# Performance work log

Hardware: AMD Instinct MI355X
Metric: run time of the kernel (lower is better)

Reference implementation:

```python
import jax, jax.numpy as jnp
import numpy as np
from jax import lax

EMBED_DIM = 128
N_RELATIONS = 64
N_ENTITIES = 100000
N_EDGES = 600000


def setup_inputs() -> dict:
    key = jax.random.key(0)
    k1, k2, k3, k4, k5, k6 = jax.random.split(key, 6)
    entity_emb = jax.random.normal(k1, (N_ENTITIES, EMBED_DIM), dtype=jnp.float32)
    heads = jax.random.randint(k2, (N_EDGES,), 0, N_ENTITIES)
    rels = jax.random.randint(k3, (N_EDGES,), 0, N_RELATIONS)
    tails = jax.random.randint(k4, (N_EDGES,), 0, N_ENTITIES)
    # learned params: relation embedding table (std=0.01) and square Linear weight (xavier)
    rel_embed_weight = 0.01 * jax.random.normal(k5, (N_RELATIONS, EMBED_DIM), dtype=jnp.float32)
    xavier = float(np.sqrt(6.0 / (EMBED_DIM + EMBED_DIM)))
    W = jax.random.uniform(k6, (EMBED_DIM, EMBED_DIM), dtype=jnp.float32, minval=-xavier, maxval=xavier)
    return {"entity_emb": entity_emb, "rel_embed_weight": rel_embed_weight, "W": W,
            "heads": heads, "rels": rels, "tails": tails}


def reference(entity_emb, rel_embed_weight, W, heads, rels, tails):
    n_entities = entity_emb.shape[0]
    # gather edge endpoint / relation embeddings: [E, D]
    e_h = entity_emb[heads]
    e_t = entity_emb[tails]
    e_r = rel_embed_weight[rels]
    # tanh-gated dot-product score per edge: [E]
    score = jnp.sum(e_t * jnp.tanh(e_h + e_r), axis=-1)
    # global max-shift (detached in torch) then per-head segment softmax
    score_exp = jnp.exp(score - lax.stop_gradient(jnp.max(score)))
    score_sum = jax.ops.segment_sum(score_exp, heads, num_segments=n_entities)
    attn = score_exp / (score_sum[heads] + 1e-10)
    # scatter-add attention-weighted messages back to head nodes: [N, D]
    agg = jax.ops.segment_sum(attn[:, None] * e_t, heads, num_segments=n_entities)
    # final Linear (no bias) + LeakyReLU(0.2); dropout is identity in eval mode
    out = (entity_emb + agg) @ W.T
    return jax.nn.leaky_relu(out, negative_slope=0.2)
```

## Files before the change

### kernel.cpp

```cpp
#include <hip/hip_runtime.h>
#include <math.h>

#define EMBED 128
#define BMAX 8192
#define LDSPAD 136
#define DBINS 64

#define TWO_LOG2E 2.8853900817779268f
#define DEFER_THR 32.0f

typedef __attribute__((ext_vector_type(8))) short short8;
typedef __attribute__((ext_vector_type(4))) float floatx4;

__device__ __forceinline__ float ex2(float x) { return __builtin_amdgcn_exp2f(x); }

__device__ __forceinline__ float fast_tanh2(float x) {
    float e = ex2(TWO_LOG2E * x);
    return 1.0f - 2.0f * __builtin_amdgcn_rcpf(1.0f + e);
}

__device__ __forceinline__ unsigned short f2b(float f) {
    union { float f; unsigned int u; } v; v.f = f;
    unsigned int r = v.u + 0x7FFFu + ((v.u >> 16) & 1u);
    return (unsigned short)(r >> 16);
}

__device__ __forceinline__ float b2f(short u) {
    union { float f; unsigned int i; } v;
    v.i = ((unsigned int)(unsigned short)u) << 16;
    return v.f;
}

template <int CTRL>
__device__ __forceinline__ float dpp_add_f(float x) {
    int y = __builtin_amdgcn_update_dpp(0, __float_as_int(x), CTRL, 0xF, 0xF, false);
    return x + __int_as_float(y);
}
__device__ __forceinline__ float dpp_sum16(float s) {
    s = dpp_add_f<0x121>(s);
    s = dpp_add_f<0x122>(s);
    s = dpp_add_f<0x124>(s);
    s = dpp_add_f<0x128>(s);
    return s;
}

__global__ __launch_bounds__(256) void k_cast_hist(
    const float* __restrict__ ent, const float* __restrict__ rel, const float* __restrict__ W,
    short* __restrict__ entb, short* __restrict__ relb, short* __restrict__ wb,
    const int* __restrict__ heads, int* __restrict__ cnt, int* __restrict__ ghist,
    int ngE, int ngR, int ngW, int E)
{
    if (blockIdx.x == 0 && threadIdx.x < DBINS) ghist[threadIdx.x] = 0;
    int stride = gridDim.x * 256;
    int total = ngE + ngR + ngW;
    for (int g = blockIdx.x * 256 + threadIdx.x; g < total; g += stride) {
        const float4* src; short* dst;
        if (g < ngE)            { src = (const float4*)ent + (size_t)g * 2;              dst = entb + (size_t)g * 8; }
        else if (g < ngE + ngR) { int g2 = g - ngE;       src = (const float4*)rel + (size_t)g2 * 2; dst = relb + (size_t)g2 * 8; }
        else                    { int g2 = g - ngE - ngR; src = (const float4*)W   + (size_t)g2 * 2; dst = wb   + (size_t)g2 * 8; }
        float4 a = src[0], b = src[1];
        short8 o;
        o[0] = (short)f2b(a.x); o[1] = (short)f2b(a.y); o[2] = (short)f2b(a.z); o[3] = (short)f2b(a.w);
        o[4] = (short)f2b(b.x); o[5] = (short)f2b(b.y); o[6] = (short)f2b(b.z); o[7] = (short)f2b(b.w);
        *(short8*)dst = o;
    }
    for (int e = blockIdx.x * 256 + threadIdx.x; e < E; e += stride)
        atomicAdd(cnt + heads[e], 1);
}

__global__ __launch_bounds__(1024) void k_scan1(
    const int* __restrict__ cnt, int* __restrict__ offs,
    int* __restrict__ bsum, int* __restrict__ ghist, int N)
{
    __shared__ int wsum[16];
    __shared__ int dh[DBINS];
    const int tid = threadIdx.x;
    if (tid < DBINS) dh[tid] = 0;
    int i = blockIdx.x * 1024 + tid;
    int v = (i < N) ? cnt[i] : 0;
    __syncthreads();
    if (i < N) atomicAdd(&dh[v < DBINS ? v : DBINS - 1], 1);
    int x = v;
    #pragma unroll
    for (int d = 1; d < 64; d <<= 1) {
        int y = __shfl_up(x, d, 64);
        if ((tid & 63) >= d) x += y;
    }
    if ((tid & 63) == 63) wsum[tid >> 6] = x;
    __syncthreads();
    if (tid < 16) {
        int w = wsum[tid];
        #pragma unroll
        for (int d = 1; d < 16; d <<= 1) {
            int y = __shfl_up(w, d, 16);
            if (tid >= d) w += y;
        }
        wsum[tid] = w;
    }
    __syncthreads();
    int add = (tid >= 64) ? wsum[(tid >> 6) - 1] : 0;
    int incl = x + add;
    if (i < N) offs[i] = incl - v;
    if (tid == 1023) bsum[blockIdx.x] = incl;
    if (tid < DBINS && dh[tid] > 0) atomicAdd(ghist + tid, dh[tid]);
}

__global__ __launch_bounds__(256) void k_scan23(
    int* __restrict__ offs, const int* __restrict__ bsum,
    int* __restrict__ cursor, const int* __restrict__ cnt,
    const int* __restrict__ ghist, int* __restrict__ bincur,
    int* __restrict__ order, int N, int nb)
{
    __shared__ int sb[256];
    __shared__ int ws4[4];
    __shared__ int dbs[DBINS];
    __shared__ int lcnt[DBINS];
    __shared__ int lbase[DBINS];
    const int tid = threadIdx.x;

    int v = (tid < nb) ? bsum[tid] : 0;
    int x = v;
    #pragma unroll
    for (int d = 1; d < 64; d <<= 1) {
        int y = __shfl_up(x, d, 64);
        if ((tid & 63) >= d) x += y;
    }
    if ((tid & 63) == 63) ws4[tid >> 6] = x;
    __syncthreads();
    if (tid < 4) {
        int w = ws4[tid];
        #pragma unroll
        for (int d = 1; d < 4; d <<= 1) {
            int y = __shfl_up(w, d, 4);
            if (tid >= d) w += y;
        }
        ws4[tid] = w;
    }
    __syncthreads();
    int add = (tid >= 64) ? ws4[(tid >> 6) - 1] : 0;
    sb[tid] = x + add - v;

    if (tid < 64) {
        int g = ghist[tid];
        int s = g;
        #pragma unroll
        for (int d = 1; d < 64; d <<= 1) {
            int y = __shfl_up(s, d, 64);
            if (tid >= d) s += y;
        }
        dbs[tid] = s - g;
    }
    if (tid < DBINS) lcnt[tid] = 0;
    __syncthreads();

    int i = blockIdx.x * 256 + tid;
    int deg = 0, lrank = 0;
    if (i < N) {
        int o = offs[i] + sb[i >> 10];
        offs[i] = o;
        cursor[i] = o;
        int c = cnt[i];
        deg = c < DBINS ? c : DBINS - 1;
        lrank = atomicAdd(&lcnt[deg], 1);
    }
    __syncthreads();
    if (tid < DBINS) {
        int n = lcnt[tid];
        lbase[tid] = (n > 0) ? (dbs[tid] + atomicAdd(bincur + tid, n)) : 0;
    }
    __syncthreads();
    if (i < N) order[lbase[deg] + lrank] = i;
}

__global__ __launch_bounds__(256) void k_csr(
    const int* __restrict__ heads, const int* __restrict__ rels,
    const int* __restrict__ tails, int* __restrict__ cursor,
    int2* __restrict__ tr, int E)
{
    int e = blockIdx.x * 256 + threadIdx.x;
    if (e >= E) return;
    int pos = atomicAdd(cursor + heads[e], 1);
    tr[pos] = make_int2(tails[e], rels[e]);
}

__global__ __launch_bounds__(256) void k_fused(
    const short* __restrict__ entb, const short* __restrict__ relb,
    const int* __restrict__ offs, const int* __restrict__ cnt,
    const int2* __restrict__ tr, const int* __restrict__ order,
    short* __restrict__ accb, float* __restrict__ mh, float* __restrict__ lh,
    float* __restrict__ blockmax, int N, int R)
{
    __shared__ short rl[64 * EMBED];
    const int tid = threadIdx.x;
    if (R <= 64) {
        int nch = R * 16;
        for (int i = tid; i < nch; i += 256)
            ((short8*)rl)[i] = ((const short8*)relb)[i];
    }
    __syncthreads();
    const short* relsrc = (R <= 64) ? (const short*)rl : relb;

    const int lane = tid & 15;
    int head0 = blockIdx.x * 16 + (tid >> 4);
    int head  = (head0 < N) ? order[head0] : N;
    float mt = -INFINITY;
    if (head < N) {
        int start = offs[head];
        int c     = cnt[head];
        short8 hh = *((const short8*)(entb + (size_t)head * EMBED) + lane);
        float hf[8];
        #pragma unroll
        for (int i = 0; i < 8; ++i) hf[i] = b2f(hh[i]);
        float m = -INFINITY;
        float l = 0.f;
        float acc[8] = {0,0,0,0,0,0,0,0};
        for (int base = 0; base < c; base += 16) {
            int rem = c - base;
            int mm  = rem < 16 ? rem : 16;
            int2 trv = make_int2(0, 0);
            if (lane < mm) trv = tr[start + base + lane];
            for (int j = 0; j < mm; ++j) {
                int t = __shfl(trv.x, j, 16);
                int r = __shfl(trv.y, j, 16);
                short8 vt = *((const short8*)(entb + (size_t)t * EMBED) + lane);
                short8 vr = *((const short8*)(relsrc + (size_t)r * EMBED) + lane);
                float s = 0.f;
                float vtf[8];
                #pragma unroll
                for (int i = 0; i < 8; ++i) {
                    vtf[i] = b2f(vt[i]);
                    s = fmaf(vtf[i], fast_tanh2(hf[i] + b2f(vr[i])), s);
                }
                s = dpp_sum16(s);
                mt = fmaxf(mt, s);
                float dlt = s - m;
                if (dlt > DEFER_THR) {
                    float alpha = __expf(-dlt);
                    l *= alpha;
                    #pragma unroll
                    for (int q = 0; q < 8; ++q) acc[q] *= alpha;
                    m = s;
                    dlt = 0.f;
                }
                float p = __expf(dlt);
                l += p;
                #pragma unroll
                for (int q = 0; q < 8; ++q)
                    acc[q] = fmaf(p, vtf[q], acc[q]);
            }
        }
        short8 o;
        #pragma unroll
        for (int q = 0; q < 8; ++q) o[q] = (short)f2b(acc[q]);
        *((short8*)(accb + (size_t)head * EMBED) + lane) = o;
        if (lane == 0) { mh[head] = m; lh[head] = l; }
    }
    __shared__ float smax[256];
    smax[tid] = mt;
    __syncthreads();
    for (int off = 128; off > 0; off >>= 1) {
        if (tid < off) smax[tid] = fmaxf(smax[tid], smax[tid + off]);
        __syncthreads();
    }
    if (tid == 0) blockmax[blockIdx.x] = smax[0];
}

__global__ __launch_bounds__(256) void k_maxred(
    const float* __restrict__ blockmax, float* __restrict__ Mout, int n)
{
    __shared__ float smax[256];
    float m = -INFINITY;
    for (int i = threadIdx.x; i < n; i += 256) m = fmaxf(m, blockmax[i]);
    smax[threadIdx.x] = m;
    __syncthreads();
    for (int off = 128; off > 0; off >>= 1) {
        if ((int)threadIdx.x < off)
            smax[threadIdx.x] = fmaxf(smax[threadIdx.x], smax[threadIdx.x + off]);
        __syncthreads();
    }
    if (threadIdx.x == 0) Mout[0] = smax[0];
}

__global__ __launch_bounds__(256) void k_gemm_f(
    const short* __restrict__ entb, const short* __restrict__ accb,
    const float* __restrict__ mh, const float* __restrict__ lh,
    const float* __restrict__ Mptr, const short* __restrict__ wb,
    float* __restrict__ out, int N)
{
    __shared__ short xs[128 * LDSPAD];
    __shared__ short ws[128 * LDSPAD];
    __shared__ float invs[128];
    const int tid = threadIdx.x;
    const int n0  = blockIdx.x * 128;
    const float M = Mptr[0];

    if (tid < 128) {
        int g = n0 + tid;
        invs[tid] = (g < N) ? 1.0f / (lh[g] + 1e-10f * __expf(M - mh[g])) : 0.f;
    }
    #pragma unroll
    for (int it = 0; it < 8; ++it) {
        int ch = it * 256 + tid;
        int row = ch >> 4, col8 = ch & 15;
        *(short8*)(ws + row * LDSPAD + col8 * 8) = ((const short8*)wb)[ch];
    }
    __syncthreads();
    #pragma unroll
    for (int it = 0; it < 8; ++it) {
        int ch = it * 256 + tid;
        int row = ch >> 4, col8 = ch & 15;
        int g = n0 + row;
        short8 v = {0,0,0,0,0,0,0,0};
        if (g < N) {
            float inv = invs[row];
            short8 e8 = *((const short8*)(entb + (size_t)g * EMBED) + col8);
            short8 a8 = *((const short8*)(accb + (size_t)g * EMBED) + col8);
            #pragma unroll
            for (int q = 0; q < 8; ++q)
                v[q] = (short)f2b(b2f(e8[q]) + b2f(a8[q]) * inv);
        }
        *(short8*)(xs + row * LDSPAD + col8 * 8) = v;
    }
    __syncthreads();

    const int wv   = tid >> 6;
    const int lane = tid & 63;
    const int n16  = lane & 15;
    const int quad = lane >> 4;

    floatx4 acc[2][8];
    #pragma unroll
    for (int rt = 0; rt < 2; ++rt)
        #pragma unroll
        for (int jt = 0; jt < 8; ++jt)
            acc[rt][jt] = (floatx4){0.f, 0.f, 0.f, 0.f};

    #pragma unroll
    for (int kc = 0; kc < 4; ++kc) {
        int koff = kc * 32 + quad * 8;
        short8 a0 = *(const short8*)(xs + (wv * 32      + n16) * LDSPAD + koff);
        short8 a1 = *(const short8*)(xs + (wv * 32 + 16 + n16) * LDSPAD + koff);
        #pragma unroll
        for (int jt = 0; jt < 8; ++jt) {
            short8 b = *(const short8*)(ws + (jt * 16 + n16) * LDSPAD + koff);
            acc[0][jt] = __builtin_amdgcn_mfma_f32_16x16x32_bf16(a0, b, acc[0][jt], 0, 0, 0);
            acc[1][jt] = __builtin_amdgcn_mfma_f32_16x16x32_bf16(a1, b, acc[1][jt], 0, 0, 0);
        }
    }

    #pragma unroll
    for (int rt = 0; rt < 2; ++rt) {
        int rowbase = n0 + wv * 32 + rt * 16 + quad * 4;
        #pragma unroll
        for (int r = 0; r < 4; ++r) {
            int grow = rowbase + r;
            if (grow < N) {
                float* o = out + (size_t)grow * EMBED + n16;
                #pragma unroll
                for (int jt = 0; jt < 8; ++jt) {
                    float v = acc[rt][jt][r];
                    o[jt * 16] = (v > 0.f) ? v : 0.2f * v;
                }
            }
        }
    }
}

extern "C" void kernel_launch(void* const* d_in, const int* in_sizes, int n_in,
                              void* d_out, int out_size, void* d_ws, size_t ws_size,
                              hipStream_t stream)
{
    const float* ent   = (const float*)d_in[0];
    const float* rel   = (const float*)d_in[1];
    const float* W     = (const float*)d_in[2];
    const int*   heads = (const int*)d_in[3];
    const int*   rels  = (const int*)d_in[4];
    const int*   tails = (const int*)d_in[5];
    const int E = in_sizes[3];
    const int N = in_sizes[0] / EMBED;
    const int R = in_sizes[1] / EMBED;
    float* out = (float*)d_out;

    short* accb     = (short*)d_ws;
    float* mh       = (float*)(accb + (size_t)N * EMBED);
    float* lh       = mh + N;
    int2*  tr       = (int2*)(lh + N);
    int*   cnt      = (int*)(tr + E);
    int*   bincur   = cnt + N;
    int*   offs     = bincur + DBINS;
    int*   cursor   = offs + N;
    float* blockmax = (float*)(cursor + N);
    float* Mval     = blockmax + BMAX;
    int*   bsum     = (int*)(Mval + 4);
    int*   ghist    = bsum + 1024;
    int*   order    = ghist + DBINS;
    short* wb       = (short*)(order + N);
    short* entb     = wb + 16384;
    short* relb     = entb + (size_t)N * EMBED;

    const int nb  = (N + 1023) >> 10;
    const int ngh = (N + 15) / 16;

    hipMemsetAsync(cnt, 0, (size_t)(N + DBINS) * sizeof(int), stream);

    int ngE = N * EMBED / 8, ngR = R * EMBED / 8, ngW = EMBED * EMBED / 8;
    k_cast_hist<<<2048, 256, 0, stream>>>(ent, rel, W, entb, relb, wb, heads, cnt, ghist, ngE, ngR, ngW, E);
    k_scan1<<<nb, 1024, 0, stream>>>(cnt, offs, bsum, ghist, N);
    k_scan23<<<(N + 255) / 256, 256, 0, stream>>>(offs, bsum, cursor, cnt, ghist, bincur, order, N, nb);
    k_csr<<<(E + 255) / 256, 256, 0, stream>>>(heads, rels, tails, cursor, tr, E);
    k_fused<<<ngh, 256, 0, stream>>>(entb, relb, offs, cnt, tr, order, accb, mh, lh, blockmax, N, R);
    k_maxred<<<1, 256, 0, stream>>>(blockmax, Mval, ngh);
    k_gemm_f<<<(N + 127) / 128, 256, 0, stream>>>(entb, accb, mh, lh, Mval, wb, out, N);
}
```

Measured before the change: 242.5 us.

## Prefetch next edge rows, drop LDS relation table, and use wave-shuffle block max

The fused edge kernel now software-pipelines its gather loop: it loads the tail and relation rows for edge j+1 while computing edge j, so global-load latency overlaps the tanh and softmax arithmetic. The LDS copy of the relation table and its barrier are removed, and relation rows are read straight from global memory, which saves LDS and may raise occupancy. The block-max reduction becomes a wave-level xor shuffle plus a 4-entry shared array instead of a log-step LDS tree with many barriers. Heads are also processed in reverse of the order array, which changes how degree-sorted work is assigned to blocks. In exchange it holds extra registers for the prefetched rows and issues one redundant load on the last edge of each chunk.

```diff
diff --git a/kernel.cpp b/kernel.cpp
--- a/kernel.cpp
+++ b/kernel.cpp
@@ -190,19 +190,10 @@
     short* __restrict__ accb, float* __restrict__ mh, float* __restrict__ lh,
     float* __restrict__ blockmax, int N, int R)
 {
-    __shared__ short rl[64 * EMBED];
     const int tid = threadIdx.x;
-    if (R <= 64) {
-        int nch = R * 16;
-        for (int i = tid; i < nch; i += 256)
-            ((short8*)rl)[i] = ((const short8*)relb)[i];
-    }
-    __syncthreads();
-    const short* relsrc = (R <= 64) ? (const short*)rl : relb;
-
     const int lane = tid & 15;
     int head0 = blockIdx.x * 16 + (tid >> 4);
-    int head  = (head0 < N) ? order[head0] : N;
+    int head  = (head0 < N) ? order[(N - 1) - head0] : N;
     float mt = -INFINITY;
     if (head < N) {
         int start = offs[head];
@@ -219,17 +210,22 @@
             int mm  = rem < 16 ? rem : 16;
             int2 trv = make_int2(0, 0);
             if (lane < mm) trv = tr[start + base + lane];
+            int t0 = __shfl(trv.x, 0, 16);
+            int r0 = __shfl(trv.y, 0, 16);
+            short8 vtc = *((const short8*)(entb + (size_t)t0 * EMBED) + lane);
+            short8 vrc = *((const short8*)(relb + (size_t)r0 * EMBED) + lane);
             for (int j = 0; j < mm; ++j) {
-                int t = __shfl(trv.x, j, 16);
-                int r = __shfl(trv.y, j, 16);
-                short8 vt = *((const short8*)(entb + (size_t)t * EMBED) + lane);
-                short8 vr = *((const short8*)(relsrc + (size_t)r * EMBED) + lane);
+                int jn = (j + 1 < mm) ? j + 1 : j;
+                int tn = __shfl(trv.x, jn, 16);
+                int rn = __shfl(trv.y, jn, 16);
+                short8 vtn = *((const short8*)(entb + (size_t)tn * EMBED) + lane);
+                short8 vrn = *((const short8*)(relb + (size_t)rn * EMBED) + lane);
                 float s = 0.f;
                 float vtf[8];
                 #pragma unroll
                 for (int i = 0; i < 8; ++i) {
-                    vtf[i] = b2f(vt[i]);
-                    s = fmaf(vtf[i], fast_tanh2(hf[i] + b2f(vr[i])), s);
+                    vtf[i] = b2f(vtc[i]);
+                    s = fmaf(vtf[i], fast_tanh2(hf[i] + b2f(vrc[i])), s);
                 }
                 s = dpp_sum16(s);
                 mt = fmaxf(mt, s);
@@ -247,6 +243,8 @@
                 #pragma unroll
                 for (int q = 0; q < 8; ++q)
                     acc[q] = fmaf(p, vtf[q], acc[q]);
+                vtc = vtn;
+                vrc = vrn;
             }
         }
         short8 o;
@@ -255,14 +253,14 @@
         *((short8*)(accb + (size_t)head * EMBED) + lane) = o;
         if (lane == 0) { mh[head] = m; lh[head] = l; }
     }
-    __shared__ float smax[256];
-    smax[tid] = mt;
-    __syncthreads();
-    for (int off = 128; off > 0; off >>= 1) {
-        if (tid < off) smax[tid] = fmaxf(smax[tid], smax[tid + off]);
-        __syncthreads();
-    }
-    if (tid == 0) blockmax[blockIdx.x] = smax[0];
+    __shared__ float wmax[4];
+    float wm = mt;
+    #pragma unroll
+    for (int off = 1; off < 64; off <<= 1) wm = fmaxf(wm, __shfl_xor(wm, off, 64));
+    if ((tid & 63) == 0) wmax[tid >> 6] = wm;
+    __syncthreads();
+    if (tid == 0)
+        blockmax[blockIdx.x] = fmaxf(fmaxf(wmax[0], wmax[1]), fmaxf(wmax[2], wmax[3]));
 }
 
 __global__ __launch_bounds__(256) void k_maxred(
```

After: 238.5 us. About the same (-1.6%).
